# Kernel tuning notes

Measured on AMD Instinct MI355X. Metric: run time of the kernel, lower is better.

## Reference

```python
import jax, jax.numpy as jnp
import numpy as np

N_NODES = 100000
N_EDGES = 3200000
IN_CH = 32
OUT_CH = 32
DIM = 2
KSIZE = 3  # per pseudo dimension -> num_kernels = 9


def setup_inputs() -> dict:
    key = jax.random.key(0)
    k1, k2, k3, k4, k5, k6 = jax.random.split(key, 6)
    x = jax.random.normal(k1, (N_NODES, IN_CH), dtype=jnp.float32)
    pseudo = jax.random.uniform(k2, (N_EDGES, DIM), dtype=jnp.float32)
    weight = jax.random.normal(k3, (KSIZE * KSIZE, IN_CH, OUT_CH), dtype=jnp.float32) / np.sqrt(IN_CH)
    root_w = jax.random.normal(k4, (OUT_CH, IN_CH), dtype=jnp.float32) / np.sqrt(IN_CH)
    root_b = jax.random.normal(k5, (OUT_CH,), dtype=jnp.float32) * 0.01
    edge_index = jax.random.randint(k6, (2, N_EDGES), 0, N_NODES, dtype=jnp.int64)
    return {"x": x, "pseudo": pseudo, "weight": weight, "root_w": root_w,
            "root_b": root_b, "edge_index": edge_index}


def _basis(pseudo):
    # degree-1 B-spline (hat) basis per dim, outer product across dims -> [E, K^dim]
    p = jnp.clip(pseudo, 0.0, 1.0)  # [E, dim]
    grid = jnp.linspace(0.0, 1.0, KSIZE, dtype=p.dtype)  # [K]
    dist = jnp.abs(p[:, :, None] - grid[None, None, :])  # [E, dim, K]
    b = jnp.maximum(1.0 - dist * (KSIZE - 1), 0.0)  # [E, dim, K]
    basis = jnp.einsum('ea,eb->eab', b[:, 0], b[:, 1])  # [E, K, K]
    return basis.reshape(p.shape[0], -1)  # [E, K*K]


def reference(x, pseudo, weight, root_w, root_b, edge_index):
    row, col = edge_index[0], edge_index[1]
    basis = _basis(pseudo)  # [E, K]
    # gather + basis-weighted contraction -> per-edge messages [E, out]
    messages = jnp.einsum('ek,ei,kio->eo', basis, x[row], weight)
    out = jnp.zeros((x.shape[0], weight.shape[2]), dtype=x.dtype).at[col].add(messages)
    # mean aggregation: divide by in-degree (clamped to >= 1)
    degree = jnp.zeros((x.shape[0],), dtype=x.dtype).at[col].add(jnp.ones_like(col, dtype=x.dtype))
    out = out / jnp.maximum(degree, 1.0)[:, None]
    # root linear (torch nn.Linear: x @ W.T + b)
    out = out + x @ root_w.T + root_b
    return out
```

## Files before the change

kernel.cpp:

```cpp
#include <hip/hip_runtime.h>
#include <hip/hip_bf16.h>

#define N_NODES 100000
#define N_EDGES 3200000
#define CH 32
#define NK 9
#define KTOT 320
#define RS 328

#define BNODES 128
#define NBUCK ((N_NODES + BNODES - 1) / BNODES)
#define CURS_PAD 16
#define MAXB 4800
#define CHE 8192
#define NCHUNK ((N_EDGES + CHE - 1) / CHE)

typedef __hip_bfloat16 bf16;
typedef unsigned short u16;
typedef __attribute__((ext_vector_type(8))) short bf16x8;
typedef __attribute__((ext_vector_type(4))) float f32x4;

__global__ __launch_bounds__(256) void prep_kernel(const float* __restrict__ x,
                                                   const float* __restrict__ w,
                                                   const float* __restrict__ rw,
                                                   bf16* __restrict__ xb,
                                                   bf16* __restrict__ Bg) {
    int idx = blockIdx.x * 256 + threadIdx.x;
    if (idx < N_NODES * CH / 4) {
        float4 v = ((const float4*)x)[idx];
        union { bf16 h[4]; uint2 u; } pk;
        pk.h[0] = __float2bfloat16(v.x);
        pk.h[1] = __float2bfloat16(v.y);
        pk.h[2] = __float2bfloat16(v.z);
        pk.h[3] = __float2bfloat16(v.w);
        ((uint2*)xb)[idx] = pk.u;
    }
    if (idx < NK * CH * CH) {
        int kk = idx >> 5, o = idx & 31;
        Bg[o * RS + kk] = __float2bfloat16(w[idx]);
    }
    if (idx < CH * CH) {
        int o = idx >> 5, i = idx & 31;
        Bg[o * RS + 288 + i] = __float2bfloat16(rw[idx]);
    }
}

__global__ __launch_bounds__(256) void bhist_kernel(const int* __restrict__ ei_col,
                                                    int* __restrict__ hist) {
    __shared__ int h[NBUCK];
    for (int j = threadIdx.x; j < NBUCK; j += 256) h[j] = 0;
    __syncthreads();
    const int4* c4 = (const int4*)ei_col;
    int stride = gridDim.x * 256;
    for (int e = blockIdx.x * 256 + threadIdx.x; e < N_EDGES / 4; e += stride) {
        int4 v = c4[e];
        atomicAdd(&h[v.x >> 7], 1);
        atomicAdd(&h[v.y >> 7], 1);
        atomicAdd(&h[v.z >> 7], 1);
        atomicAdd(&h[v.w >> 7], 1);
    }
    __syncthreads();
    for (int j = threadIdx.x; j < NBUCK; j += 256)
        if (h[j]) atomicAdd(&hist[j], h[j]);
}

__global__ __launch_bounds__(1024) void bscan_kernel(const int* __restrict__ hist,
                                                     int* __restrict__ bstart,
                                                     int* __restrict__ cursor) {
    __shared__ int s[1024];
    int t = threadIdx.x;
    int a = (2 * t < NBUCK) ? hist[2 * t] : 0;
    int b = (2 * t + 1 < NBUCK) ? hist[2 * t + 1] : 0;
    s[t] = a + b;
    __syncthreads();
    for (int off = 1; off < 1024; off <<= 1) {
        int u = (t >= off) ? s[t - off] : 0;
        __syncthreads();
        s[t] += u;
        __syncthreads();
    }
    int excl = s[t] - (a + b);
    if (2 * t < NBUCK) {
        bstart[2 * t] = excl;
        cursor[2 * t * CURS_PAD] = excl;
    }
    if (2 * t + 1 < NBUCK) {
        bstart[2 * t + 1] = excl + a;
        cursor[(2 * t + 1) * CURS_PAD] = excl + a;
    }
    if (t == 1023) bstart[NBUCK] = s[1023];
}

__global__ __launch_bounds__(1024) void place_kernel(const float* __restrict__ pseudo,
                                                     const int* __restrict__ ei,
                                                     int* __restrict__ cursor,
                                                     uint2* __restrict__ edata) {
    __shared__ uint2 buf[CHE];
    __shared__ unsigned inv[CHE];
    __shared__ int h[NBUCK];
    __shared__ int loff[NBUCK];
    __shared__ int gb[NBUCK];
    __shared__ int cur[NBUCK];
    __shared__ int tps[1024];
    int tid = threadIdx.x;
    int c0 = blockIdx.x * CHE;
    int cend = min(c0 + CHE, N_EDGES);
    int sz = cend - c0;

    for (int j = tid; j < NBUCK; j += 1024) h[j] = 0;
    __syncthreads();
    for (int e = c0 + tid; e < cend; e += 1024) {
        int col = ei[N_EDGES + e];
        int row = ei[e];
        float2 pp = ((const float2*)pseudo)[e];
        float pa = fminf(fmaxf(pp.x, 0.f), 1.f);
        float pb = fminf(fmaxf(pp.y, 0.f), 1.f);
        int ia = pa < 0.5f ? 0 : 1;
        int ib = pb < 0.5f ? 0 : 1;
        float wa1 = 2.f * (pa - 0.5f * (float)ia);
        float wb1 = 2.f * (pb - 0.5f * (float)ib);
        unsigned qa = (unsigned)(wa1 * 65535.f + 0.5f);
        unsigned qb = (unsigned)(wb1 * 65535.f + 0.5f);
        uint2 d;
        d.x = (unsigned)row | ((unsigned)ia << 17) | ((unsigned)ib << 18)
            | ((unsigned)(col & 127) << 20);
        d.y = qa | (qb << 16);
        buf[e - c0] = d;
        atomicAdd(&h[col >> 7], 1);
    }
    __syncthreads();
    int v = (tid < NBUCK) ? h[tid] : 0;
    tps[tid] = v;
    __syncthreads();
    for (int d = 1; d < 1024; d <<= 1) {
        int u = (tid >= d) ? tps[tid - d] : 0;
        __syncthreads();
        tps[tid] += u;
        __syncthreads();
    }
    if (tid < NBUCK) {
        int excl = tps[tid] - v;
        loff[tid] = excl;
        cur[tid] = excl;
        gb[tid] = v ? atomicAdd(&cursor[tid * CURS_PAD], v) : 0;
    }
    __syncthreads();
    for (int e = c0 + tid; e < cend; e += 1024) {
        int b = ei[N_EDGES + e] >> 7;
        int p = atomicAdd(&cur[b], 1);
        inv[p] = (unsigned)(e - c0) | ((unsigned)b << 13);
    }
    __syncthreads();
    for (int q = tid; q < sz; q += 1024) {
        unsigned u = inv[q];
        int b = (int)(u >> 13);
        uint2 rec = buf[u & 8191];
        edata[gb[b] + (q - loff[b])] = rec;
    }
}

__global__ __launch_bounds__(256) void bsort_kernel(const int* __restrict__ bstart,
                                                    uint2* __restrict__ edata,
                                                    int* __restrict__ nstart,
                                                    int* __restrict__ ncnt) {
    __shared__ uint2 buf[MAXB];
    __shared__ int h[BNODES];
    __shared__ int cur[BNODES];
    __shared__ int tp[256];
    int tid = threadIdx.x;
    int b = blockIdx.x;
    int e0 = bstart[b], e1 = bstart[b + 1];
    int sz = min(e1 - e0, MAXB);

    if (tid < BNODES) h[tid] = 0;
    for (int j = tid; j < sz; j += 256) buf[j] = edata[e0 + j];
    __syncthreads();
    for (int j = tid; j < sz; j += 256)
        atomicAdd(&h[(buf[j].x >> 20) & 127], 1);
    __syncthreads();
    int v = (tid < BNODES) ? h[tid] : 0;
    tp[tid] = v;
    __syncthreads();
    for (int d = 1; d < 256; d <<= 1) {
        int u = (tid >= d) ? tp[tid - d] : 0;
        __syncthreads();
        tp[tid] += u;
        __syncthreads();
    }
    int excl = tp[tid] - v;
    if (tid < BNODES) {
        cur[tid] = excl;
        int n = b * BNODES + tid;
        if (n < N_NODES) { nstart[n] = e0 + excl; ncnt[n] = v; }
    }
    __syncthreads();
    for (int j = tid; j < sz; j += 256) {
        uint2 r = buf[j];
        unsigned xx = r.x;
        int key = (xx >> 20) & 127;
        int p = atomicAdd(&cur[key], 1);
        float wa1f = (float)(r.y & 0xFFFF) * (1.f / 65535.f);
        float wb1f = (float)(r.y >> 16) * (1.f / 65535.f);
        unsigned wa1b = __float_as_uint(wa1f) >> 16;
        unsigned wb1b = __float_as_uint(wb1f) >> 16;
        uint2 outr;
        outr.x = ((xx & 0x1FFFF) << 6)
               | ((xx & (1u << 17)) << 13)
               | ((xx & (1u << 18)) << 13);
        outr.y = wa1b | (wb1b << 16);
        edata[e0 + p] = outr;
    }
}

__global__ __launch_bounds__(256, 6) void gather_mm_kernel(const bf16* __restrict__ xb,
                                                           const bf16* __restrict__ Bg,
                                                           const float* __restrict__ rb,
                                                           const int* __restrict__ nstart,
                                                           const int* __restrict__ ncnt,
                                                           const uint2* __restrict__ edata,
                                                           float* __restrict__ out) {
    __shared__ __align__(16) bf16 zlds[16 * RS];
    __shared__ __align__(16) bf16 coef[4][16 * 40];
    __shared__ __align__(16) bf16 xt[4][32 * 36];
    int tid = threadIdx.x;
    int wid = tid >> 6;
    int lane = tid & 63;
    int lr = lane & 15, lg = lane >> 4;
    int e31 = lane & 31;
    int n0 = blockIdx.x * 16;
    const char* xbb = (const char*)xb;

    bf16* coefW = coef[wid];
    u16* xtU = (u16*)xt[wid];

    {
        int* cz = (int*)coefW;
        for (int j = lane; j < 16 * 40 / 2; j += 64) cz[j] = 0;
    }

    for (int s = 0; s < 4; ++s) {
        int rr = wid * 4 + s;
        int n = n0 + rr;
        int s0 = nstart[n];
        int dg = ncnt[n];
        f32x4 accL = {0.f, 0.f, 0.f, 0.f};
        f32x4 accH = {0.f, 0.f, 0.f, 0.f};
        int ng = (dg + 31) >> 5;

        for (int g = 0; g < ng; ++g) {
            uint2 rec = edata[s0 + g * 32 + e31];
            bool valid = (g * 32 + e31) < dg;
            float wa1 = __uint_as_float(rec.y << 16);
            float wb1 = __uint_as_float(rec.y & 0xFFFF0000u);
            wa1 = valid ? wa1 : 0.f;
            wb1 = valid ? wb1 : 0.f;
            float wa0 = 1.f - wa1, wb0 = 1.f - wb1;
            unsigned rx = rec.x;
            int ia = (rx >> 30) & 1;
            int ib = (rx >> 31) & 1;
            float A0 = ia ? 0.f : wa0, A1 = ia ? wa0 : wa1, A2 = ia ? wa1 : 0.f;
            float B0 = ib ? 0.f : wb0, B1 = ib ? wb0 : wb1, B2 = ib ? wb1 : 0.f;
            A0 = valid ? A0 : 0.f;
            A1 = valid ? A1 : 0.f;
            A2 = valid ? A2 : 0.f;
            int ro = valid ? (int)(rx & 0x00FFFFC0u) : 0;

            if (lane < 32) {
                coefW[0 * 40 + e31] = __float2bfloat16(A0 * B0);
                coefW[1 * 40 + e31] = __float2bfloat16(A0 * B1);
                coefW[2 * 40 + e31] = __float2bfloat16(A0 * B2);
                coefW[3 * 40 + e31] = __float2bfloat16(A1 * B0);
                coefW[4 * 40 + e31] = __float2bfloat16(A1 * B1);
                coefW[5 * 40 + e31] = __float2bfloat16(A1 * B2);
                coefW[6 * 40 + e31] = __float2bfloat16(A2 * B0);
                coefW[7 * 40 + e31] = __float2bfloat16(A2 * B1);
                coefW[8 * 40 + e31] = __float2bfloat16(A2 * B2);
            }

            int rem = dg - g * 32;
#pragma unroll
            for (int t = 0; t < 2; ++t) {
                int e = 16 * t + (lane >> 2);
                int roe = __shfl(ro, e);
                uint4 v = *(const uint4*)(xbb + roe + (lane & 3) * 16);
                bool vx = e < rem;
                v.x = vx ? v.x : 0u;
                v.y = vx ? v.y : 0u;
                v.z = vx ? v.z : 0u;
                v.w = vx ? v.w : 0u;
                int c0 = (lane & 3) * 8;
                xtU[(c0 + 0) * 36 + e] = (u16)(v.x);
                xtU[(c0 + 1) * 36 + e] = (u16)(v.x >> 16);
                xtU[(c0 + 2) * 36 + e] = (u16)(v.y);
                xtU[(c0 + 3) * 36 + e] = (u16)(v.y >> 16);
                xtU[(c0 + 4) * 36 + e] = (u16)(v.z);
                xtU[(c0 + 5) * 36 + e] = (u16)(v.z >> 16);
                xtU[(c0 + 6) * 36 + e] = (u16)(v.w);
                xtU[(c0 + 7) * 36 + e] = (u16)(v.w >> 16);
            }

            bf16x8 af = *(const bf16x8*)(coefW + lr * 40 + lg * 8);
            const uint2* xlo = (const uint2*)((const char*)xtU + lr * 72 + lg * 16);
            const uint2* xhi = (const uint2*)((const char*)xtU + (lr + 16) * 72 + lg * 16);
            uint2 l0 = xlo[0], l1 = xlo[1];
            uint2 h0 = xhi[0], h1 = xhi[1];
            union UB { unsigned w[4]; bf16x8 v; } bl, bh;
            bl.w[0] = l0.x; bl.w[1] = l0.y; bl.w[2] = l1.x; bl.w[3] = l1.y;
            bh.w[0] = h0.x; bh.w[1] = h0.y; bh.w[2] = h1.x; bh.w[3] = h1.y;
            accL = __builtin_amdgcn_mfma_f32_16x16x32_bf16(af, bl.v, accL, 0, 0, 0);
            accH = __builtin_amdgcn_mfma_f32_16x16x32_bf16(af, bh.v, accH, 0, 0, 0);
        }

        float inv = 1.f / fmaxf((float)dg, 1.f);
#pragma unroll
        for (int r = 0; r < 4; ++r) {
            int p = lg * 4 + r;
            if (p < 9) {
                zlds[rr * RS + p * 32 + lr]      = __float2bfloat16(accL[r] * inv);
                zlds[rr * RS + p * 32 + lr + 16] = __float2bfloat16(accH[r] * inv);
            }
        }
        if (lane < CH) zlds[rr * RS + 288 + lane] = xb[(size_t)n * CH + lane];
    }
    __syncthreads();

    if (wid < 2) {
        const bf16* brow = Bg + (size_t)(lr + wid * 16) * RS;
        f32x4 acc = {0.f, 0.f, 0.f, 0.f};
#pragma unroll
        for (int ks = 0; ks < 10; ++ks) {
            int kk = ks * 32 + lg * 8;
            bf16x8 a = *(const bf16x8*)(zlds + lr * RS + kk);
            bf16x8 b = *(const bf16x8*)(brow + kk);
            acc = __builtin_amdgcn_mfma_f32_16x16x32_bf16(a, b, acc, 0, 0, 0);
        }
        float bias = rb[lr + wid * 16];
#pragma unroll
        for (int r = 0; r < 4; ++r) {
            int n = n0 + lg * 4 + r;
            out[(size_t)n * CH + lr + wid * 16] = acc[r] + bias;
        }
    }
}

extern "C" void kernel_launch(void* const* d_in, const int* in_sizes, int n_in,
                              void* d_out, int out_size, void* d_ws, size_t ws_size,
                              hipStream_t stream) {
    const float* x      = (const float*)d_in[0];
    const float* pseudo = (const float*)d_in[1];
    const float* weight = (const float*)d_in[2];
    const float* root_w = (const float*)d_in[3];
    const float* root_b = (const float*)d_in[4];
    const int*   ei     = (const int*)d_in[5];
    float* out = (float*)d_out;

    int* hist    = (int*)d_ws;
    int* bstart  = hist + 1024;
    int* cursor  = bstart + 1024;
    int* nstart  = cursor + 12544;
    int* ncnt    = nstart + 100032;
    char* basep  = (char*)(ncnt + 100032);
    size_t off   = ((size_t)(basep - (char*)d_ws) + 1023) & ~(size_t)1023;
    uint2* edata = (uint2*)((char*)d_ws + off);
    bf16* xb     = (bf16*)(edata + N_EDGES + 64);
    bf16* Bg     = xb + (size_t)N_NODES * CH;

    hipMemsetAsync(hist, 0, NBUCK * sizeof(int), stream);
    prep_kernel<<<(N_NODES * CH / 4 + 255) / 256, 256, 0, stream>>>(x, weight, root_w, xb, Bg);
    bhist_kernel<<<256, 256, 0, stream>>>(ei + N_EDGES, hist);
    bscan_kernel<<<1, 1024, 0, stream>>>(hist, bstart, cursor);
    place_kernel<<<NCHUNK, 1024, 0, stream>>>(pseudo, ei, cursor, edata);
    bsort_kernel<<<NBUCK, 256, 0, stream>>>(bstart, edata, nstart, ncnt);
    gather_mm_kernel<<<N_NODES / 16, 256, 0, stream>>>(xb, Bg, root_b, nstart, ncnt,
                                                       edata, out);
}
```

Baseline: 158.2 us.

## Interleave two nodes per wave with edge-record prefetch and packed LDS transpose

Each wave now processes two destination nodes at once, each with its own coef/xt LDS buffers, so the gathers for both nodes are issued before either is consumed. The edge record for the next group is prefetched one iteration ahead. The x transpose into LDS now uses lane-pair shuffles to write packed 32-bit words instead of 16-bit scalar stores. Together these aim to raise memory-level parallelism and hide gather latency. In exchange the kernel uses more registers and LDS, so the occupancy hint is lowered from 6 to 4, and waves stall on the slower of each node pair.

```diff
diff --git a/kernel.cpp b/kernel.cpp
--- a/kernel.cpp
+++ b/kernel.cpp
@@ -212,7 +212,7 @@
     }
 }
 
-__global__ __launch_bounds__(256, 6) void gather_mm_kernel(const bf16* __restrict__ xb,
+__global__ __launch_bounds__(256, 4) void gather_mm_kernel(const bf16* __restrict__ xb,
                                                            const bf16* __restrict__ Bg,
                                                            const float* __restrict__ rb,
                                                            const int* __restrict__ nstart,
@@ -220,8 +220,8 @@
                                                            const uint2* __restrict__ edata,
                                                            float* __restrict__ out) {
     __shared__ __align__(16) bf16 zlds[16 * RS];
-    __shared__ __align__(16) bf16 coef[4][16 * 40];
-    __shared__ __align__(16) bf16 xt[4][32 * 36];
+    __shared__ __align__(16) bf16 coef[8][16 * 40];
+    __shared__ __align__(16) bf16 xt[8][32 * 36];
     int tid = threadIdx.x;
     int wid = tid >> 6;
     int lane = tid & 63;
@@ -229,98 +229,168 @@
     int e31 = lane & 31;
     int n0 = blockIdx.x * 16;
     const char* xbb = (const char*)xb;
-
-    bf16* coefW = coef[wid];
-    u16* xtU = (u16*)xt[wid];
+    bool evenlane = (lane & 4) == 0;
+
+    bf16* coefA = coef[wid * 2];
+    bf16* coefB = coef[wid * 2 + 1];
+    u16* xtUA = (u16*)xt[wid * 2];
+    u16* xtUB = (u16*)xt[wid * 2 + 1];
+    unsigned* x32A = (unsigned*)xt[wid * 2];
+    unsigned* x32B = (unsigned*)xt[wid * 2 + 1];
+
+    union UBu { unsigned w[4]; bf16x8 v; };
 
     {
-        int* cz = (int*)coefW;
-        for (int j = lane; j < 16 * 40 / 2; j += 64) cz[j] = 0;
-    }
-
-    for (int s = 0; s < 4; ++s) {
-        int rr = wid * 4 + s;
-        int n = n0 + rr;
-        int s0 = nstart[n];
-        int dg = ncnt[n];
-        f32x4 accL = {0.f, 0.f, 0.f, 0.f};
-        f32x4 accH = {0.f, 0.f, 0.f, 0.f};
-        int ng = (dg + 31) >> 5;
-
-        for (int g = 0; g < ng; ++g) {
-            uint2 rec = edata[s0 + g * 32 + e31];
-            bool valid = (g * 32 + e31) < dg;
-            float wa1 = __uint_as_float(rec.y << 16);
-            float wb1 = __uint_as_float(rec.y & 0xFFFF0000u);
-            wa1 = valid ? wa1 : 0.f;
-            wb1 = valid ? wb1 : 0.f;
-            float wa0 = 1.f - wa1, wb0 = 1.f - wb1;
-            unsigned rx = rec.x;
-            int ia = (rx >> 30) & 1;
-            int ib = (rx >> 31) & 1;
-            float A0 = ia ? 0.f : wa0, A1 = ia ? wa0 : wa1, A2 = ia ? wa1 : 0.f;
-            float B0 = ib ? 0.f : wb0, B1 = ib ? wb0 : wb1, B2 = ib ? wb1 : 0.f;
-            A0 = valid ? A0 : 0.f;
-            A1 = valid ? A1 : 0.f;
-            A2 = valid ? A2 : 0.f;
-            int ro = valid ? (int)(rx & 0x00FFFFC0u) : 0;
-
-            if (lane < 32) {
-                coefW[0 * 40 + e31] = __float2bfloat16(A0 * B0);
-                coefW[1 * 40 + e31] = __float2bfloat16(A0 * B1);
-                coefW[2 * 40 + e31] = __float2bfloat16(A0 * B2);
-                coefW[3 * 40 + e31] = __float2bfloat16(A1 * B0);
-                coefW[4 * 40 + e31] = __float2bfloat16(A1 * B1);
-                coefW[5 * 40 + e31] = __float2bfloat16(A1 * B2);
-                coefW[6 * 40 + e31] = __float2bfloat16(A2 * B0);
-                coefW[7 * 40 + e31] = __float2bfloat16(A2 * B1);
-                coefW[8 * 40 + e31] = __float2bfloat16(A2 * B2);
+        int* czA = (int*)coefA;
+        int* czB = (int*)coefB;
+        for (int j = lane; j < 16 * 40 / 2; j += 64) { czA[j] = 0; czB[j] = 0; }
+    }
+
+#define G_DECODE(REC, G, DG, A0_,A1_,A2_,B0_,B1_,B2_, RO_)                    \
+    {                                                                         \
+        bool valid = ((G) * 32 + e31) < (DG);                                 \
+        float wa1 = __uint_as_float((REC).y << 16);                           \
+        float wb1 = __uint_as_float((REC).y & 0xFFFF0000u);                   \
+        wa1 = valid ? wa1 : 0.f;                                              \
+        wb1 = valid ? wb1 : 0.f;                                              \
+        float wa0 = 1.f - wa1, wb0 = 1.f - wb1;                               \
+        unsigned rx = (REC).x;                                                \
+        int ia = (rx >> 30) & 1, ib = (rx >> 31) & 1;                         \
+        A0_ = ia ? 0.f : wa0; A1_ = ia ? wa0 : wa1; A2_ = ia ? wa1 : 0.f;     \
+        B0_ = ib ? 0.f : wb0; B1_ = ib ? wb0 : wb1; B2_ = ib ? wb1 : 0.f;     \
+        A0_ = valid ? A0_ : 0.f;                                              \
+        A1_ = valid ? A1_ : 0.f;                                              \
+        A2_ = valid ? A2_ : 0.f;                                              \
+        RO_ = valid ? (int)(rx & 0x00FFFFC0u) : 0;                            \
+    }
+
+#define G_LOAD(RO_, V0_, V1_)                                                 \
+    {                                                                         \
+        int roe0 = __shfl((RO_), lane >> 2);                                  \
+        int roe1 = __shfl((RO_), 16 + (lane >> 2));                           \
+        V0_ = *(const uint4*)(xbb + roe0 + (lane & 3) * 16);                  \
+        V1_ = *(const uint4*)(xbb + roe1 + (lane & 3) * 16);                  \
+    }
+
+#define G_COEF(COEFW, A0_,A1_,A2_,B0_,B1_,B2_)                                \
+    if (lane < 32) {                                                          \
+        (COEFW)[0 * 40 + e31] = __float2bfloat16(A0_ * B0_);                  \
+        (COEFW)[1 * 40 + e31] = __float2bfloat16(A0_ * B1_);                  \
+        (COEFW)[2 * 40 + e31] = __float2bfloat16(A0_ * B2_);                  \
+        (COEFW)[3 * 40 + e31] = __float2bfloat16(A1_ * B0_);                  \
+        (COEFW)[4 * 40 + e31] = __float2bfloat16(A1_ * B1_);                  \
+        (COEFW)[5 * 40 + e31] = __float2bfloat16(A1_ * B2_);                  \
+        (COEFW)[6 * 40 + e31] = __float2bfloat16(A2_ * B0_);                  \
+        (COEFW)[7 * 40 + e31] = __float2bfloat16(A2_ * B1_);                  \
+        (COEFW)[8 * 40 + e31] = __float2bfloat16(A2_ * B2_);                  \
+    }
+
+#define G_XPUT(X32, V_, T, REM)                                               \
+    {                                                                         \
+        int e = 16 * (T) + (lane >> 2);                                       \
+        uint4 v = (V_);                                                       \
+        bool vx = e < (REM);                                                  \
+        v.x = vx ? v.x : 0u;                                                  \
+        v.y = vx ? v.y : 0u;                                                  \
+        v.z = vx ? v.z : 0u;                                                  \
+        v.w = vx ? v.w : 0u;                                                  \
+        unsigned s0v = evenlane ? v.z : v.x;                                  \
+        unsigned s1v = evenlane ? v.w : v.y;                                  \
+        unsigned r0 = __shfl_xor(s0v, 4);                                     \
+        unsigned r1 = __shfl_xor(s1v, 4);                                     \
+        unsigned Ae = evenlane ? v.x : r0;                                    \
+        unsigned Bo = evenlane ? r0 : v.z;                                    \
+        unsigned Ce = evenlane ? v.y : r1;                                    \
+        unsigned Do = evenlane ? r1 : v.w;                                    \
+        int a = (lane & 3) * 8 + (evenlane ? 0 : 4);                          \
+        int sl = 8 * (T) + (lane >> 3);                                       \
+        (X32)[(a + 0) * 18 + sl] = (Ae & 0xFFFFu) | (Bo << 16);               \
+        (X32)[(a + 1) * 18 + sl] = (Ae >> 16) | (Bo & 0xFFFF0000u);           \
+        (X32)[(a + 2) * 18 + sl] = (Ce & 0xFFFFu) | (Do << 16);               \
+        (X32)[(a + 3) * 18 + sl] = (Ce >> 16) | (Do & 0xFFFF0000u);           \
+    }
+
+#define G_MFMA(COEFW, XTU, ACCL, ACCH)                                        \
+    {                                                                         \
+        bf16x8 af = *(const bf16x8*)((COEFW) + lr * 40 + lg * 8);             \
+        const uint2* xlo = (const uint2*)((const char*)(XTU) + lr * 72 + lg * 16); \
+        const uint2* xhi = (const uint2*)((const char*)(XTU) + (lr + 16) * 72 + lg * 16); \
+        uint2 l0 = xlo[0], l1 = xlo[1];                                       \
+        uint2 h0 = xhi[0], h1 = xhi[1];                                       \
+        UBu bl, bh;                                                           \
+        bl.w[0] = l0.x; bl.w[1] = l0.y; bl.w[2] = l1.x; bl.w[3] = l1.y;       \
+        bh.w[0] = h0.x; bh.w[1] = h0.y; bh.w[2] = h1.x; bh.w[3] = h1.y;       \
+        ACCL = __builtin_amdgcn_mfma_f32_16x16x32_bf16(af, bl.v, ACCL, 0, 0, 0); \
+        ACCH = __builtin_amdgcn_mfma_f32_16x16x32_bf16(af, bh.v, ACCH, 0, 0, 0); \
+    }
+
+#define G_EPI(RR, N, DG, ACCL, ACCH)                                          \
+    {                                                                         \
+        float inv = 1.f / fmaxf((float)(DG), 1.f);                            \
+        _Pragma("unroll")                                                     \
+        for (int r = 0; r < 4; ++r) {                                         \
+            int p = lg * 4 + r;                                               \
+            if (p < 9) {                                                      \
+                zlds[(RR) * RS + p * 32 + lr]      = __float2bfloat16(ACCL[r] * inv); \
+                zlds[(RR) * RS + p * 32 + lr + 16] = __float2bfloat16(ACCH[r] * inv); \
+            }                                                                 \
+        }                                                                     \
+        if (lane < CH) zlds[(RR) * RS + 288 + lane] = xb[(size_t)(N) * CH + lane]; \
+    }
+
+    for (int sp = 0; sp < 2; ++sp) {
+        int rrA = wid * 4 + sp * 2;
+        int rrB = rrA + 1;
+        int nA = n0 + rrA, nB = n0 + rrB;
+        int s0A = nstart[nA], dgA = ncnt[nA];
+        int s0B = nstart[nB], dgB = ncnt[nB];
+        int ngA = (dgA + 31) >> 5, ngB = (dgB + 31) >> 5;
+        int ngM = max(ngA, ngB);
+        f32x4 aLA = {0.f, 0.f, 0.f, 0.f}, aHA = {0.f, 0.f, 0.f, 0.f};
+        f32x4 aLB = {0.f, 0.f, 0.f, 0.f}, aHB = {0.f, 0.f, 0.f, 0.f};
+        uint2 recA = make_uint2(0u, 0u), recB = make_uint2(0u, 0u);
+        if (ngA) recA = edata[s0A + e31];
+        if (ngB) recB = edata[s0B + e31];
+
+        for (int g = 0; g < ngM; ++g) {
+            bool actA = g < ngA, actB = g < ngB;
+            uint2 nxA = recA, nxB = recB;
+            if (g + 1 < ngA) nxA = edata[s0A + (g + 1) * 32 + e31];
+            if (g + 1 < ngB) nxB = edata[s0B + (g + 1) * 32 + e31];
+
+            float A0a, A1a, A2a, B0a, B1a, B2a;
+            float A0b, A1b, A2b, B0b, B1b, B2b;
+            int roA = 0, roB = 0;
+            uint4 vA0, vA1, vB0, vB1;
+
+            if (actA) {
+                G_DECODE(recA, g, dgA, A0a, A1a, A2a, B0a, B1a, B2a, roA)
+                G_LOAD(roA, vA0, vA1)
             }
-
-            int rem = dg - g * 32;
-#pragma unroll
-            for (int t = 0; t < 2; ++t) {
-                int e = 16 * t + (lane >> 2);
-                int roe = __shfl(ro, e);
-                uint4 v = *(const uint4*)(xbb + roe + (lane & 3) * 16);
-                bool vx = e < rem;
-                v.x = vx ? v.x : 0u;
-                v.y = vx ? v.y : 0u;
-                v.z = vx ? v.z : 0u;
-                v.w = vx ? v.w : 0u;
-                int c0 = (lane & 3) * 8;
-                xtU[(c0 + 0) * 36 + e] = (u16)(v.x);
-                xtU[(c0 + 1) * 36 + e] = (u16)(v.x >> 16);
-                xtU[(c0 + 2) * 36 + e] = (u16)(v.y);
-                xtU[(c0 + 3) * 36 + e] = (u16)(v.y >> 16);
-                xtU[(c0 + 4) * 36 + e] = (u16)(v.z);
-                xtU[(c0 + 5) * 36 + e] = (u16)(v.z >> 16);
-                xtU[(c0 + 6) * 36 + e] = (u16)(v.w);
-                xtU[(c0 + 7) * 36 + e] = (u16)(v.w >> 16);
+            if (actB) {
+                G_DECODE(recB, g, dgB, A0b, A1b, A2b, B0b, B1b, B2b, roB)
+                G_LOAD(roB, vB0, vB1)
             }
-
-            bf16x8 af = *(const bf16x8*)(coefW + lr * 40 + lg * 8);
-            const uint2* xlo = (const uint2*)((const char*)xtU + lr * 72 + lg * 16);
-            const uint2* xhi = (const uint2*)((const char*)xtU + (lr + 16) * 72 + lg * 16);
-            uint2 l0 = xlo[0], l1 = xlo[1];
-            uint2 h0 = xhi[0], h1 = xhi[1];
-            union UB { unsigned w[4]; bf16x8 v; } bl, bh;
-            bl.w[0] = l0.x; bl.w[1] = l0.y; bl.w[2] = l1.x; bl.w[3] = l1.y;
-            bh.w[0] = h0.x; bh.w[1] = h0.y; bh.w[2] = h1.x; bh.w[3] = h1.y;
-            accL = __builtin_amdgcn_mfma_f32_16x16x32_bf16(af, bl.v, accL, 0, 0, 0);
-            accH = __builtin_amdgcn_mfma_f32_16x16x32_bf16(af, bh.v, accH, 0, 0, 0);
+            if (actA) {
+                G_COEF(coefA, A0a, A1a, A2a, B0a, B1a, B2a)
+                int remA = dgA - g * 32;
+                G_XPUT(x32A, vA0, 0, remA)
+                G_XPUT(x32A, vA1, 1, remA)
+            }
+            if (actB) {
+                G_COEF(coefB, A0b, A1b, A2b, B0b, B1b, B2b)
+                int remB = dgB - g * 32;
+                G_XPUT(x32B, vB0, 0, remB)
+                G_XPUT(x32B, vB1, 1, remB)
+            }
+            if (actA) G_MFMA(coefA, xtUA, aLA, aHA)
+            if (actB) G_MFMA(coefB, xtUB, aLB, aHB)
+            recA = nxA;
+            recB = nxB;
         }
 
-        float inv = 1.f / fmaxf((float)dg, 1.f);
-#pragma unroll
-        for (int r = 0; r < 4; ++r) {
-            int p = lg * 4 + r;
-            if (p < 9) {
-                zlds[rr * RS + p * 32 + lr]      = __float2bfloat16(accL[r] * inv);
-                zlds[rr * RS + p * 32 + lr + 16] = __float2bfloat16(accH[r] * inv);
-            }
-        }
-        if (lane < CH) zlds[rr * RS + 288 + lane] = xb[(size_t)n * CH + lane];
+        G_EPI(rrA, nA, dgA, aLA, aHA)
+        G_EPI(rrB, nB, dgB, aLB, aHB)
     }
     __syncthreads();
 
```

New measurement: 162.2 us. 2.5% more time.
